# Performance work log

Measured on AMD Instinct MI355X. Metric: run time of the kernel, lower is better.

## Reference

```python
import jax, jax.numpy as jnp
import numpy as np
from jax import lax

# encoder config from the module: (out_ch, kernel, stride), 3x3, padding=1 (pytlib ConvolutionStack)
_LAYERS = [(3, 3, 2), (16, 3, 2), (64, 3, 1), (128, 3, 2), (256, 3, 1)]
_DN = ('NCHW', 'OIHW', 'NCHW')


def _make_params(key):
    params = []
    in_ch = 3
    for i, (out_ch, k, _s) in enumerate(_LAYERS):
        kw, kb = jax.random.split(jax.random.fold_in(key, i))
        fan_in = in_ch * k * k
        W = jax.random.normal(kw, (out_ch, in_ch, k, k), jnp.float32) * np.sqrt(2.0 / fan_in)
        b = jnp.zeros((out_ch,), jnp.float32)
        params.append((W, b))
        in_ch = out_ch
    return params


def _encoder(x, W0, b0, W1, b1, W2, b2, W3, b3, W4, b4):
    Ws = (W0, W1, W2, W3, W4)
    bs = (b0, b1, b2, b3, b4)
    for i, (_oc, _k, s) in enumerate(_LAYERS):
        x = lax.conv_general_dilated(x, Ws[i], (s, s), ((1, 1), (1, 1)), dimension_numbers=_DN)
        x = x + bs[i][None, :, None, None]
        if i < len(_LAYERS) - 1:  # final_relu=False
            x = jax.nn.relu(x)
    return x


def setup_inputs() -> dict:
    key = jax.random.key(0)
    k1, k2, kp = jax.random.split(key, 3)
    crop = jax.random.normal(k1, (64, 3, 64, 64), jnp.float32)
    frame = jax.random.normal(k2, (64, 3, 256, 256), jnp.float32)
    params = _make_params(kp)
    out = {'crop': crop, 'frame': frame}
    for i, (W, b) in enumerate(params):
        out[f'W{i}'] = W
        out[f'b{i}'] = b
    out['gamma'] = jnp.ones((1,), jnp.float32)
    out['beta'] = jnp.zeros((1,), jnp.float32)
    return out


def reference(crop, frame, W0, b0, W1, b1, W2, b2, W3, b3, W4, b4, gamma, beta):
    crop_fm = _encoder(crop, W0, b0, W1, b1, W2, b2, W3, b3, W4, b4)   # [B,256,8,8]
    frame_fm = _encoder(frame, W0, b0, W1, b1, W2, b2, W3, b3, W4, b4)  # [B,256,32,32]

    # per-sample cross-correlation: crop feature map is the conv kernel (vectorized over batch)
    def xcorr(f, k):  # f:[C,H,W], k:[C,h,w] -> [1,Hr,Wr]
        return lax.conv_general_dilated(f[None], k[None], (1, 1), 'VALID', dimension_numbers=_DN)[0]

    rmap = jax.vmap(xcorr)(frame_fm, crop_fm)  # [B,1,25,25]

    # BatchNorm2d(1), training mode: batch stats over (N,H,W), biased variance, eps=1e-5
    mean = jnp.mean(rmap, axis=(0, 2, 3), keepdims=True)
    var = jnp.mean(jnp.square(rmap - mean), axis=(0, 2, 3), keepdims=True)
    rmap = (rmap - mean) * lax.rsqrt(var + 1e-5)
    rmap = rmap * gamma[None, :, None, None] + beta[None, :, None, None]
    return rmap
```

## Files before the change

### kernel.cpp

```cpp
#include <hip/hip_runtime.h>


typedef __bf16 bf16x8 __attribute__((ext_vector_type(8)));
typedef float f32x4 __attribute__((ext_vector_type(4)));
typedef unsigned int u32x4 __attribute__((ext_vector_type(4)));
typedef unsigned int u32x2 __attribute__((ext_vector_type(2)));
typedef unsigned short u16;

#define AS1 __attribute__((address_space(1)))
#define AS3 __attribute__((address_space(3)))

__device__ __forceinline__ u16 f2bf(float v) {
    unsigned u = __float_as_uint(v);
    u += 0x7fffu + ((u >> 16) & 1u);
    return (u16)(u >> 16);
}

__device__ __forceinline__ bf16x8 ldb8(const u16* p) {
    return *(const bf16x8*)p;
}

__device__ __forceinline__ bf16x8 zerob8() {
    u32x4 z = {0u, 0u, 0u, 0u};
    bf16x8 r;
    __builtin_memcpy(&r, &z, 16);
    return r;
}

__device__ __forceinline__ void gload16(const u16* g, u16* l) {
    __builtin_amdgcn_global_load_lds((const AS1 void*)g, (AS3 void*)l, 16, 0, 0);
}

template<int N> __device__ __forceinline__ void wait_vm() {
    asm volatile("s_waitcnt vmcnt(%0)" :: "i"(N) : "memory");
}

__device__ __forceinline__ void bar_mem() {
    asm volatile("" ::: "memory");
    __builtin_amdgcn_s_barrier();
    asm volatile("" ::: "memory");
}

struct CP { const u16* in; u16* out; int IWp, inSS, OWsh, OWpo, outSS, npt; };
struct CQ { const u16* in; u16* out; int IWp, inSS, HWsh, OWsh, OWpo, outSS, pad_o; };

struct HZd { unsigned long long ptr; int B, Hp, Wpx, w8, cum; };
struct HZall { HZd d[8]; int total; };

__global__ __launch_bounds__(256)
void haloz_k(HZall h)
{
    for (int i = blockIdx.x * 256 + threadIdx.x; i < h.total; i += gridDim.x * 256) {
        int di = 0;
        #pragma unroll
        for (int j = 1; j < 8; ++j) if (i >= h.d[j].cum) di = j;
        const HZd D = h.d[di];
        const int loc = i - D.cum;
        const int w = loc % D.w8; int t2 = loc / D.w8;
        const int bord = 2 * D.Wpx + 2 * (D.Hp - 2);
        const int pb = t2 % bord; const int b = t2 / bord;
        int oh, ow;
        if (pb < D.Wpx)            { oh = 0;        ow = pb; }
        else if (pb < 2 * D.Wpx)   { oh = D.Hp - 1; ow = pb - D.Wpx; }
        else { const int q = pb - 2 * D.Wpx; oh = 1 + (q >> 1); ow = (q & 1) ? (D.Wpx - 1) : 0; }
        ((unsigned long long*)D.ptr)[((size_t)b * D.Hp * D.Wpx + (size_t)oh * D.Wpx + ow) * D.w8 + w] = 0ull;
    }
}

__device__ __forceinline__ void packone(const float* W, u16* Wp, int idx,
                                        int ICsh, int Kpad)
{
    const int k = idx % Kpad, oc = idx / Kpad;
    const int tap = k >> ICsh, ic = k & ((1 << ICsh) - 1);
    const float v = (tap < 9) ? W[((size_t)(oc << ICsh) + ic) * 9 + tap] : 0.f;
    Wp[idx] = f2bf(v);
}

__global__ __launch_bounds__(256)
void packall_k(const float* __restrict__ W1, const float* __restrict__ W2,
               const float* __restrict__ W3, const float* __restrict__ W4,
               u16* __restrict__ Wc1, u16* __restrict__ Wp2,
               u16* __restrict__ Wp3, u16* __restrict__ Wp4)
{
    const int i = blockIdx.x * 256 + threadIdx.x;
    if (i < 1024) {
        const int k = i & 63, oc = i >> 6;
        const int ky = k >> 4, kx = (k >> 2) & 3, ic = k & 3;
        const float v = (ky < 3 && kx < 3 && ic < 3) ? W1[oc * 27 + ic * 9 + ky * 3 + kx] : 0.f;
        Wc1[i] = f2bf(v);
    } else if (i < 11264) {
        packone(W2, Wp2, i - 1024, 4, 160);
    } else if (i < 84992) {
        packone(W3, Wp3, i - 11264, 6, 576);
    } else if (i < 379904) {
        packone(W4, Wp4, i - 84992, 7, 1152);
    }
}

__device__ __forceinline__ void conv0_body(const float* __restrict__ in,
                                           const float* __restrict__ W,
                                           const float* __restrict__ bias,
                                           u16* __restrict__ outP,
                                           int IH, int IW, int OH, int OW, int idx)
{
    const int OW4 = OW >> 2;
    const int OWp = OW + 2, OHp = OH + 2;
    const int ow4 = idx % OW4; int t = idx / OW4;
    const int oh = t % OH;  const int b = t / OH;
    const int owb = ow4 * 4;
    float a0[4], a1[4], a2[4];
    #pragma unroll
    for (int j = 0; j < 4; ++j) { a0[j] = bias[0]; a1[j] = bias[1]; a2[j] = bias[2]; }
    const float* inb = in + (size_t)b * 3 * IH * IW;
    const int xbase = owb * 2 - 1;
    #pragma unroll
    for (int ic = 0; ic < 3; ++ic) {
        const float* ip = inb + (size_t)ic * IH * IW;
        #pragma unroll
        for (int ky = 0; ky < 3; ++ky) {
            const int y = oh * 2 - 1 + ky;
            if ((unsigned)y >= (unsigned)IH) continue;
            const float* rp = ip + (size_t)y * IW;
            float xr[9];
            #pragma unroll
            for (int i2 = 0; i2 < 9; ++i2) {
                const int x = xbase + i2;
                xr[i2] = ((unsigned)x < (unsigned)IW) ? rp[x] : 0.f;
            }
            #pragma unroll
            for (int kx = 0; kx < 3; ++kx) {
                const float w0 = W[0 * 27 + ic * 9 + ky * 3 + kx];
                const float w1 = W[1 * 27 + ic * 9 + ky * 3 + kx];
                const float w2 = W[2 * 27 + ic * 9 + ky * 3 + kx];
                #pragma unroll
                for (int j = 0; j < 4; ++j) {
                    const float xv = xr[2 * j + kx];
                    a0[j] += xv * w0; a1[j] += xv * w1; a2[j] += xv * w2;
                }
            }
        }
    }
    u16* op = outP + (((size_t)b * OHp + oh + 1) * OWp + owb + 1) * 4;
    #pragma unroll
    for (int j = 0; j < 4; ++j) {
        u32x2 pk;
        pk[0] = (unsigned)f2bf(fmaxf(a0[j], 0.f)) | ((unsigned)f2bf(fmaxf(a1[j], 0.f)) << 16);
        pk[1] = (unsigned)f2bf(fmaxf(a2[j], 0.f));
        *(u32x2*)(op + j * 4) = pk;
    }
}

__global__ __launch_bounds__(256)
void conv0m_k(const float* __restrict__ crop, const float* __restrict__ frame,
              const float* __restrict__ W, const float* __restrict__ bias,
              u16* __restrict__ c0b, u16* __restrict__ f0b)
{
    if (blockIdx.x < 64)
        conv0_body(crop, W, bias, c0b, 64, 64, 32, 32, blockIdx.x * 256 + threadIdx.x);
    else
        conv0_body(frame, W, bias, f0b, 256, 256, 128, 128, (blockIdx.x - 64) * 256 + threadIdx.x);
}

__device__ __forceinline__ void conv1g_body(const u16* __restrict__ inP,
                                            const u16* __restrict__ Wc1,
                                            const float* __restrict__ bias,
                                            u16* __restrict__ outP,
                                            int IWp, int inSS, int OWp, int outSS,
                                            int OWsh, int HWsh, int w, int lane)
{
    const int lr = lane & 15, lg = lane >> 4;
    const int pxb = w * 64;
    const int OW = 1 << OWsh;

    const bf16x8 av0 = ldb8(Wc1 + lr * 64 + lg * 8);
    const bf16x8 av1 = ldb8(Wc1 + lr * 64 + 32 + lg * 8);
    const int ky0 = lg >> 1, kxb = (lg & 1) * 2;
    const int ky1 = 2 + (lg >> 1);

    f32x4 acc[4] = {};
    #pragma unroll
    for (int n = 0; n < 4; ++n) {
        const int px = pxb + n * 16 + lr;
        const int b = px >> HWsh;
        const int rem = px & ((1 << HWsh) - 1);
        const int oh = rem >> OWsh, ow = rem & (OW - 1);
        const u16* ib = inP + (size_t)b * inSS + (((size_t)(oh * 2)) * IWp + ow * 2) * 4;
        const bf16x8 bv0 = ldb8(ib + ((size_t)ky0 * IWp + kxb) * 4);
        acc[n] = __builtin_amdgcn_mfma_f32_16x16x32_bf16(av0, bv0, acc[n], 0, 0, 0);
        const bf16x8 bv1 = ldb8(ib + ((size_t)ky1 * IWp + kxb) * 4);
        acc[n] = __builtin_amdgcn_mfma_f32_16x16x32_bf16(av1, bv1, acc[n], 0, 0, 0);
    }

    const float b0 = bias[lg * 4], b1 = bias[lg * 4 + 1],
                b2 = bias[lg * 4 + 2], b3 = bias[lg * 4 + 3];
    #pragma unroll
    for (int n = 0; n < 4; ++n) {
        const int px = pxb + n * 16 + lr;
        const int b = px >> HWsh;
        const int rem = px & ((1 << HWsh) - 1);
        const int oh = rem >> OWsh, ow = rem & (OW - 1);
        const f32x4 a = acc[n];
        u32x2 pk;
        pk[0] = (unsigned)f2bf(fmaxf(a[0] + b0, 0.f)) | ((unsigned)f2bf(fmaxf(a[1] + b1, 0.f)) << 16);
        pk[1] = (unsigned)f2bf(fmaxf(a[2] + b2, 0.f)) | ((unsigned)f2bf(fmaxf(a[3] + b3, 0.f)) << 16);
        u16* op = outP + (size_t)b * outSS + (((size_t)(oh + 1)) * OWp + (ow + 1)) * 16 + lg * 4;
        *(u32x2*)op = pk;
    }
}

__global__ __launch_bounds__(256)
void conv1m_k(const u16* __restrict__ c0b, u16* __restrict__ c1p,
              const u16* __restrict__ f0b, u16* __restrict__ f1p,
              const u16* __restrict__ Wc1, const float* __restrict__ bias)
{
    const int wv = threadIdx.x >> 6, lane = threadIdx.x & 63;
    if (blockIdx.x < 64)
        conv1g_body(c0b, Wc1, bias, c1p, 34, 4624, 18, 5184, 4, 8, blockIdx.x * 4 + wv, lane);
    else
        conv1g_body(f0b, Wc1, bias, f1p, 130, 67600, 66, 69696, 6, 12, (blockIdx.x - 64) * 4 + wv, lane);
}

template<int BM, int BN, int NWM, int NWN, int S>
__global__ __launch_bounds__(512, 4)
void convq3_k(CQ F, CQ C, int splitPt, int nmt_sh,
              const u16* __restrict__ Wp, const float* __restrict__ bias,
              int IC_sh, int nt, int Kpad, int relu, int OCt)
{
    constexpr int MF = BM / (NWM * 16);
    constexpr int NF = BN / (NWN * 16);
    constexpr int AH = BM * 4 / 512;
    constexpr int BH = BN * 4 / 512;
    constexpr int WAIT  = 2 * AH + BH;
    constexpr int TAIL0 = AH + BH;
    constexpr int ASZ = 2 * 2 * BM * 4 * 8;
    constexpr int BSZ = 2 * 2 * BN * 4 * 8;

    __shared__ __align__(16) u16 SM[ASZ + BSZ];
    u16* Ab = SM;
    u16* Bb = SM + ASZ;

    const int mt  = blockIdx.x & ((1 << nmt_sh) - 1);
    const int ptg = blockIdx.x >> nmt_sh;
    CQ P; int pt;
    if (ptg < splitPt) { P = F; pt = ptg; }
    else               { P = C; pt = ptg - splitPt; }
    const int ocb = mt * BM;

    const int t    = threadIdx.x;
    const int lane = t & 63;
    const int lr   = lane & 15, lg = lane >> 4;
    const int wv   = t >> 6;
    const int wm   = wv / NWN, wn = wv % NWN;

    const int IC = 1 << IC_sh;
    const int OW = 1 << P.OWsh;
    const int HWm = (1 << P.HWsh) - 1;
    const int pxb = pt * BN;

    const u16* apg[2 * AH];
    #pragma unroll
    for (int h = 0; h < 2; ++h)
        #pragma unroll
        for (int i = 0; i < AH; ++i) {
            const int j = i * 512 + t;
            const int row = j >> 2, o = j & 3;
            const int oct = h * 4 + (o ^ ((row ^ (row >> 2)) & 3));
            apg[h * AH + i] = Wp + (size_t)(ocb + row) * Kpad + oct * 8;
        }
    const u16* bpg[2 * BH];
    #pragma unroll
    for (int h = 0; h < 2; ++h)
        #pragma unroll
        for (int i = 0; i < BH; ++i) {
            const int j = i * 512 + t;
            const int row = j >> 2, o = j & 3;
            const int oct = h * 4 + (o ^ ((row ^ (row >> 2)) & 3));
            const int px = pxb + row;
            const int b = px >> P.HWsh;
            const int rem = px & HWm;
            const int oh = rem >> P.OWsh, ow = rem & (OW - 1);
            bpg[h * BH + i] = P.in + (size_t)b * P.inSS
                            + ((size_t)(oh * S) * P.IWp + ow * S) * IC + oct * 8;
        }

    f32x4 acc[MF][NF] = {};

    auto STAGE_A = [&](int buf, int h, int kb) {
        u16* dst = Ab + (size_t)((buf * 2 + h) * BM * 4) * 8;
        #pragma unroll
        for (int i = 0; i < AH; ++i)
            gload16(apg[h * AH + i] + kb, dst + (size_t)(i * 512 + t) * 8);
    };
    auto STAGE_B = [&](int buf, int h, int kb) {
        const int tap = kb >> IC_sh;
        const int ky = (tap * 11) >> 5, kx = tap - 3 * ky;
        const size_t off = ((size_t)(ky * P.IWp + kx) << IC_sh) + (kb & (IC - 1));
        u16* dst = Bb + (size_t)((buf * 2 + h) * BN * 4) * 8;
        #pragma unroll
        for (int i = 0; i < BH; ++i)
            gload16(bpg[h * BH + i] + off, dst + (size_t)(i * 512 + t) * 8);
    };

    STAGE_A(0, 0, 0); STAGE_B(0, 0, 0); STAGE_A(0, 1, 0); STAGE_B(0, 1, 0);

    for (int ks = 0; ks < nt; ++ks) {
        const int cur = ks & 1, nxt = cur ^ 1;
        const int kb1 = (ks + 1) * 64;
        const bool pf = (ks + 1 < nt);
        bf16x8 af[MF], bf_[NF];

        #pragma unroll
        for (int kk = 0; kk < 2; ++kk) {
            if (pf) STAGE_A(nxt, kk, kb1);
            if (pf)            wait_vm<WAIT>();
            else if (kk == 0)  wait_vm<TAIL0>();
            else               wait_vm<0>();
            bar_mem();

            const u16* Abase = Ab + (size_t)((cur * 2 + kk) * BM * 4) * 8;
            const u16* Bbase = Bb + (size_t)((cur * 2 + kk) * BN * 4) * 8;
            #pragma unroll
            for (int n = 0; n < NF; ++n) {
                const int row = wn * (NF * 16) + n * 16 + lr;
                const int o = lg ^ ((row ^ (row >> 2)) & 3);
                bf_[n] = ldb8(Bbase + (size_t)(row * 4 + o) * 8);
            }
            #pragma unroll
            for (int m = 0; m < MF; ++m) {
                const int row = wm * (MF * 16) + m * 16 + lr;
                const int o = lg ^ ((row ^ (row >> 2)) & 3);
                af[m] = ldb8(Abase + (size_t)(row * 4 + o) * 8);
            }
            if (pf) STAGE_B(nxt, kk, kb1);

            __builtin_amdgcn_s_setprio(1);
            #pragma unroll
            for (int m = 0; m < MF; ++m)
                #pragma unroll
                for (int n = 0; n < NF; ++n)
                    acc[m][n] = __builtin_amdgcn_mfma_f32_16x16x32_bf16(af[m], bf_[n], acc[m][n], 0, 0, 0);
            __builtin_amdgcn_s_setprio(0);
        }
    }

    bar_mem();
    unsigned long long* SM64 = (unsigned long long*)SM;
    #pragma unroll
    for (int m = 0; m < MF; ++m) {
        const int ocl = wm * (MF * 16) + m * 16 + lg * 4;
        const float b0 = bias[ocb + ocl], b1 = bias[ocb + ocl + 1],
                    b2 = bias[ocb + ocl + 2], b3 = bias[ocb + ocl + 3];
        #pragma unroll
        for (int n = 0; n < NF; ++n) {
            const int px = wn * (NF * 16) + n * 16 + lr;
            const f32x4 a = acc[m][n];
            float v0 = a[0] + b0, v1 = a[1] + b1, v2 = a[2] + b2, v3 = a[3] + b3;
            if (relu) {
                v0 = fmaxf(v0, 0.f); v1 = fmaxf(v1, 0.f);
                v2 = fmaxf(v2, 0.f); v3 = fmaxf(v3, 0.f);
            }
            u32x2 pk;
            pk[0] = (unsigned)f2bf(v0) | ((unsigned)f2bf(v1) << 16);
            pk[1] = (unsigned)f2bf(v2) | ((unsigned)f2bf(v3) << 16);
            const int sw = ((px & 3) << 1) | ((px >> 2) & 1);
            const int u8 = (ocl >> 2) ^ (sw << 1);
            *(u32x2*)&SM64[(size_t)px * (BM / 4) + u8] = pk;
        }
    }
    bar_mem();
    constexpr int UPX16 = BM / 8;
    constexpr int NIT = BN * UPX16 / 512;
    #pragma unroll
    for (int it = 0; it < NIT; ++it) {
        const int g = it * 512 + t;
        const int px = g / UPX16;
        const int ul = g & (UPX16 - 1);
        const int sw = ((px & 3) << 1) | ((px >> 2) & 1);
        const int phys = ul ^ sw;
        const u32x4 val = *(const u32x4*)&SM[((size_t)px * UPX16 + phys) * 8];
        const int flat = pxb + px;
        const int b = flat >> P.HWsh;
        const int rem = flat & HWm;
        const int oh = rem >> P.OWsh, ow = rem & (OW - 1);
        u16* dst = P.out + (size_t)b * P.outSS
                 + (((size_t)(oh + P.pad_o)) * P.OWpo + (ow + P.pad_o)) * OCt
                 + ocb + ul * 8;
        *(u32x4*)dst = val;
    }
}

template<int BM, int BN, int NWM, int NWN, int S>
__global__ __launch_bounds__(256, 2)
void convg3_k(CP A, CP B, int split,
              const u16* __restrict__ Wp, const float* __restrict__ bias,
              int IC_sh, int pad_o, int Kreal, int nt, int Kpad, int relu, int OCtot)
{
    constexpr int MF = BM / (NWM * 16);
    constexpr int NF = BN / (NWN * 16);
    constexpr int ASLOT = BM * 4;
    constexpr int BSLOT = BN * 4;
    constexpr int AISS = ASLOT / 256;
    constexpr int BISS = BSLOT / 256;
    constexpr int NSTG = AISS + BISS;

    __shared__ __align__(16) u16 Ab[4][ASLOT * 8];
    __shared__ __align__(16) u16 Bb[4][BSLOT * 8];

    CP P; int bid;
    if (blockIdx.x < (unsigned)split) { P = A; bid = blockIdx.x; }
    else                              { P = B; bid = blockIdx.x - split; }

    const int t    = threadIdx.x;
    const int wv   = t >> 6, lane = t & 63;
    const int lr   = lane & 15, lg = lane >> 4;
    const int wm   = wv / NWN, wn = wv % NWN;

    const int tilesPerB = (OCtot / BM) * P.npt;
    const int b  = bid / tilesPerB;
    const int r0 = bid - b * tilesPerB;
    const int mt = r0 / P.npt, pt = r0 - mt * P.npt;
    const int ocb = mt * BM, pxb = pt * BN;
    const int IC = 1 << IC_sh;
    const int OW = 1 << P.OWsh;

    const u16* __restrict__ inb = P.in + (size_t)b * P.inSS;

    const u16* agp[AISS];
    #pragma unroll
    for (int i = 0; i < AISS; ++i) {
        const int s = i * 256 + t;
        const int q = s / BM, rr = s - q * BM;
        agp[i] = Wp + (size_t)(ocb + rr) * Kpad + q * 8;
    }
    int bq[BISS]; const u16* bpx[BISS];
    #pragma unroll
    for (int i = 0; i < BISS; ++i) {
        const int s = i * 256 + t;
        const int q = s / BN, rr = s - q * BN;
        const int px = pxb + rr;
        const int oh = px >> P.OWsh, ow = px & (OW - 1);
        bq[i] = q;
        bpx[i] = inb + ((size_t)(oh * S) * P.IWp + ow * S) * IC;
    }

    f32x4 acc[MF][NF] = {};

    auto STAGE = [&](int buf, int kb) {
        #pragma unroll
        for (int i = 0; i < AISS; ++i)
            gload16(agp[i] + kb, &Ab[buf][(size_t)(i * 256 + wv * 64) * 8]);
        #pragma unroll
        for (int i = 0; i < BISS; ++i) {
            const int k = kb + bq[i] * 8;
            const int tap = k >> IC_sh;
            const int ic = k & (IC - 1);
            const int ky = (tap * 11) >> 5, kx = tap - 3 * ky;
            const u16* g = bpx[i] + ((size_t)ky * P.IWp + kx) * IC + ic;
            if (k >= Kreal) g = inb;
            gload16(g, &Bb[buf][(size_t)(i * 256 + wv * 64) * 8]);
        }
    };

    STAGE(0, 0);
    if (1 < nt) STAGE(1, 32);
    if (2 < nt) STAGE(2, 64);

    for (int ks = 0; ks < nt; ++ks) {
        const int rem = nt - 1 - ks;
        if (rem >= 2)      wait_vm<2 * NSTG>();
        else if (rem == 1) wait_vm<NSTG>();
        else               wait_vm<0>();
        bar_mem();
        if (ks + 3 < nt) STAGE((ks + 3) & 3, (ks + 3) * 32);

        const int cur = ks & 3;
        bf16x8 af[MF], bf_[NF];
        #pragma unroll
        for (int m = 0; m < MF; ++m)
            af[m] = ldb8(&Ab[cur][(size_t)(lg * BM + wm * (MF * 16) + m * 16 + lr) * 8]);
        #pragma unroll
        for (int n = 0; n < NF; ++n)
            bf_[n] = ldb8(&Bb[cur][(size_t)(lg * BN + wn * (NF * 16) + n * 16 + lr) * 8]);

        __builtin_amdgcn_s_setprio(1);
        #pragma unroll
        for (int m = 0; m < MF; ++m)
            #pragma unroll
            for (int n = 0; n < NF; ++n)
                acc[m][n] = __builtin_amdgcn_mfma_f32_16x16x32_bf16(af[m], bf_[n], acc[m][n], 0, 0, 0);
        __builtin_amdgcn_s_setprio(0);
    }

    #pragma unroll
    for (int m = 0; m < MF; ++m) {
        const int oc0 = ocb + wm * (MF * 16) + m * 16 + lg * 4;
        const float b0 = bias[oc0], b1 = bias[oc0 + 1], b2 = bias[oc0 + 2], b3 = bias[oc0 + 3];
        #pragma unroll
        for (int n = 0; n < NF; ++n) {
            const int px = pxb + wn * (NF * 16) + n * 16 + lr;
            const int oh = px >> P.OWsh, ow = px & (OW - 1);
            const f32x4 a = acc[m][n];
            float v0 = a[0] + b0, v1 = a[1] + b1, v2 = a[2] + b2, v3 = a[3] + b3;
            if (relu) {
                v0 = fmaxf(v0, 0.f); v1 = fmaxf(v1, 0.f);
                v2 = fmaxf(v2, 0.f); v3 = fmaxf(v3, 0.f);
            }
            u32x2 pk;
            pk[0] = (unsigned)f2bf(v0) | ((unsigned)f2bf(v1) << 16);
            pk[1] = (unsigned)f2bf(v2) | ((unsigned)f2bf(v3) << 16);
            u16* op = P.out + (size_t)b * P.outSS +
                      (((size_t)(oh + pad_o)) * P.OWpo + (ow + pad_o)) * (size_t)OCtot + oc0;
            *(u32x2*)op = pk;
        }
    }
}

__global__ __launch_bounds__(256)
void xcmf_k(const u16* __restrict__ ffm, const u16* __restrict__ cfm,
            float* __restrict__ R)
{
    const int w    = blockIdx.x * 4 + (threadIdx.x >> 6);
    const int lane = threadIdx.x & 63;
    const int lr   = lane & 15, lg = lane >> 4;
    const int b  = w / 25;
    const int tp = w - b * 25;

    const int col0 = tp * 32 + lr;
    const int col1 = col0 + 16;
    const int y0 = col0 / 25, x0 = col0 - y0 * 25;
    const int y1 = col1 / 25, x1 = col1 - y1 * 25;

    const u16* fb = ffm + (size_t)b * 262144;
    const u16* f0 = fb + ((size_t)y0 * 32 + x0) * 256 + lg * 8;
    const u16* f1 = fb + ((size_t)y1 * 32 + x1) * 256 + lg * 8;
    const u16* ab = cfm + (size_t)b * 16384 + (size_t)lr * 2048 + lg * 8;
    const bool arow = (lr < 8);

    f32x4 acc0 = {}, acc1 = {};
    #pragma unroll 4
    for (int kb = 0; kb < 2048; kb += 32) {
        const bf16x8 av = arow ? ldb8(ab + kb) : zerob8();
        const bf16x8 bv0 = ldb8(f0 + kb);
        const bf16x8 bv1 = ldb8(f1 + kb);
        acc0 = __builtin_amdgcn_mfma_f32_16x16x32_bf16(av, bv0, acc0, 0, 0, 0);
        acc1 = __builtin_amdgcn_mfma_f32_16x16x32_bf16(av, bv1, acc1, 0, 0, 0);
    }

    if (lg < 2) {
        float* rb = R + (size_t)b * 6400;
        #pragma unroll
        for (int j = 0; j < 4; ++j) {
            const int d = lg * 4 + j;
            rb[(size_t)d * 800 + col0] = acc0[j];
            rb[(size_t)d * 800 + col1] = acc1[j];
        }
    }
}

__global__ __launch_bounds__(1024)
void bn_k(const float* __restrict__ R, float* __restrict__ part,
          const float* __restrict__ gamma, const float* __restrict__ beta,
          float* __restrict__ out)
{
    const int N = 40000;
    const int tid = threadIdx.x;
    __shared__ float rs[1024], rq[1024];
    __shared__ float mean_s, inv_s;
    float s = 0.f, q = 0.f;
    for (int i = tid; i < N; i += 1024) {
        const int b = i / 625;
        const int o = i - b * 625;
        const float* rb = R + (size_t)b * 6400 + o;
        float v = 0.f;
        #pragma unroll
        for (int d = 0; d < 8; ++d) v += rb[(size_t)d * 800 + d * 25];
        part[i] = v;
        s += v; q += v * v;
    }
    rs[tid] = s; rq[tid] = q;
    __syncthreads();
    for (int off = 512; off > 0; off >>= 1) {
        if (tid < off) { rs[tid] += rs[tid + off]; rq[tid] += rq[tid + off]; }
        __syncthreads();
    }
    if (tid == 0) {
        const float m = rs[0] / (float)N;
        mean_s = m;
        inv_s = rsqrtf(rq[0] / (float)N - m * m + 1e-5f);
    }
    __syncthreads();
    const float g = gamma[0], bt = beta[0];
    for (int i = tid; i < N; i += 1024)
        out[i] = (part[i] - mean_s) * inv_s * g + bt;
}


extern "C" void kernel_launch(void* const* d_in, const int* in_sizes, int n_in,
                              void* d_out, int out_size, void* d_ws, size_t ws_size,
                              hipStream_t stream)
{
    (void)in_sizes; (void)n_in; (void)out_size; (void)ws_size;
    const float* crop  = (const float*)d_in[0];
    const float* frame = (const float*)d_in[1];
    const float* W[5]; const float* bb[5];
    for (int i = 0; i < 5; ++i) { W[i] = (const float*)d_in[2 + 2*i]; bb[i] = (const float*)d_in[3 + 2*i]; }
    const float* gamma = (const float*)d_in[12];
    const float* beta  = (const float*)d_in[13];
    float* out = (float*)d_out;

    unsigned char* ws = (unsigned char*)d_ws;
    u16*   f0b  = (u16*)(ws + 0);
    u16*   f1p  = (u16*)(ws + 8652800);
    u16*   f2p  = (u16*)(ws + 17573888);
    u16*   f3p  = (u16*)(ws + 53258240);
    u16*   ffm  = (u16*)(ws + 0);
    u16*   c0b  = (u16*)(ws + 72198144);
    u16*   c1p  = (u16*)(ws + 72790016);
    u16*   c2p  = (u16*)(ws + 73453568);
    u16*   c3p  = (u16*)(ws + 76107776);
    u16*   cfm  = (u16*)(ws + 77746176);
    u16*   Wc1  = (u16*)(ws + 79843328);
    u16*   Wp2  = (u16*)(ws + 79845376);
    u16*   Wp3  = (u16*)(ws + 79865856);
    u16*   Wp4  = (u16*)(ws + 80013312);
    float* Rbuf = (float*)(ws + 80603136);
    float* part = (float*)(ws + 82241536);

    HZall hz;
    const unsigned long long ptrs[8] = {(unsigned long long)c0b, (unsigned long long)c1p,
        (unsigned long long)c2p, (unsigned long long)c3p, (unsigned long long)f0b,
        (unsigned long long)f1p, (unsigned long long)f2p, (unsigned long long)f3p};
    const int Hps[8] = {34, 18, 18, 10, 130, 66, 66, 34};
    const int w8s[8] = {1, 4, 16, 32, 1, 4, 16, 32};
    int cum = 0;
    for (int i = 0; i < 8; ++i) {
        hz.d[i].ptr = ptrs[i]; hz.d[i].B = 64; hz.d[i].Hp = Hps[i];
        hz.d[i].Wpx = Hps[i]; hz.d[i].w8 = w8s[i]; hz.d[i].cum = cum;
        cum += 64 * (2 * Hps[i] + 2 * (Hps[i] - 2)) * w8s[i];
    }
    hz.total = cum;
    haloz_k<<<1024, 256, 0, stream>>>(hz);

    packall_k<<<1484, 256, 0, stream>>>(W[1], W[2], W[3], W[4], Wc1, Wp2, Wp3, Wp4);

    conv0m_k<<<1088, 256, 0, stream>>>(crop, frame, W[0], bb[0], c0b, f0b);
    conv1m_k<<<1088, 256, 0, stream>>>(c0b, c1p, f0b, f1p, Wc1, bb[1]);
    {
        CP Ac = {c1p, c2p, 18,  5184, 4, 18, 20736,  1};
        CP Bf = {f1p, f2p, 66, 69696, 6, 66, 278784, 16};
        convg3_k<64,256,1,4,1><<<1088, 256, 0, stream>>>(Ac, Bf, 64, Wp2, bb[2],
            4, 1, 144, 5, 160, 1, 64);
    }

    {
        CQ F3 = {f2p, f3p, 66, 278784, 10,  5,   34,  147968, 1};
        CQ C3 = {c2p, c3p, 18,  20736,  6,  3,   10,   12800, 1};
        convq3_k<128,128,2,4,2><<< 544, 512, 0, stream>>>(F3, C3, 512, 0, Wp3, bb[3], 6,  9,  576, 1, 128);
        CQ F4 = {f3p, ffm, 34, 147968, 10,  5,   32,  262144, 0};
        CQ C4 = {c3p, cfm, 10,  12800,  6,  3,    8,   16384, 0};
        convq3_k<128,128,2,4,1><<<1088, 512, 0, stream>>>(F4, C4, 512, 1, Wp4, bb[4], 7, 18, 1152, 0, 256);
    }

    xcmf_k<<<400, 256, 0, stream>>>(ffm, cfm, Rbuf);
    bn_k<<<1, 1024, 0, stream>>>(Rbuf, part, gamma, beta, out);
}
```

Measured before the change: 230.7 us.

## Fuse prep kernels, remap blocks per XCD, swizzle LDS layout in convg

Merges the halo-zeroing and weight-packing kernels into one launch, which removes one kernel launch. Remaps block indices in the two GEMM conv kernels so that consecutive logical tiles land on the same XCD, aiming for better L2 reuse of weights and inputs. Changes the convg LDS staging layout to a row-major layout with an XOR swizzle, intended to cut LDS bank conflicts on the MFMA operand reads. The XCD remap assumes the grid size is divisible by 8, which holds for 1088 and 544.

Result: no change. 227.5 us (-1.4%).

```diff
diff --git a/kernel.cpp b/kernel.cpp
--- a/kernel.cpp
+++ b/kernel.cpp
@@ -41,16 +41,51 @@
     asm volatile("" ::: "memory");
 }
 
+__device__ __forceinline__ int xcd_logical() {
+    const int nb = (int)gridDim.x;
+    return ((int)blockIdx.x & 7) * (nb >> 3) + ((int)blockIdx.x >> 3);
+}
+
 struct CP { const u16* in; u16* out; int IWp, inSS, OWsh, OWpo, outSS, npt; };
 struct CQ { const u16* in; u16* out; int IWp, inSS, HWsh, OWsh, OWpo, outSS, pad_o; };
 
 struct HZd { unsigned long long ptr; int B, Hp, Wpx, w8, cum; };
 struct HZall { HZd d[8]; int total; };
 
+__device__ __forceinline__ void packone(const float* W, u16* Wp, int idx,
+                                        int ICsh, int Kpad)
+{
+    const int k = idx % Kpad, oc = idx / Kpad;
+    const int tap = k >> ICsh, ic = k & ((1 << ICsh) - 1);
+    const float v = (tap < 9) ? W[((size_t)(oc << ICsh) + ic) * 9 + tap] : 0.f;
+    Wp[idx] = f2bf(v);
+}
+
 __global__ __launch_bounds__(256)
-void haloz_k(HZall h)
-{
-    for (int i = blockIdx.x * 256 + threadIdx.x; i < h.total; i += gridDim.x * 256) {
+void prep_k(HZall h,
+            const float* __restrict__ W1, const float* __restrict__ W2,
+            const float* __restrict__ W3, const float* __restrict__ W4,
+            u16* __restrict__ Wc1, u16* __restrict__ Wp2,
+            u16* __restrict__ Wp3, u16* __restrict__ Wp4)
+{
+    if (blockIdx.x < 1484) {
+        const int i = blockIdx.x * 256 + threadIdx.x;
+        if (i < 1024) {
+            const int k = i & 63, oc = i >> 6;
+            const int ky = k >> 4, kx = (k >> 2) & 3, ic = k & 3;
+            const float v = (ky < 3 && kx < 3 && ic < 3) ? W1[oc * 27 + ic * 9 + ky * 3 + kx] : 0.f;
+            Wc1[i] = f2bf(v);
+        } else if (i < 11264) {
+            packone(W2, Wp2, i - 1024, 4, 160);
+        } else if (i < 84992) {
+            packone(W3, Wp3, i - 11264, 6, 576);
+        } else if (i < 379904) {
+            packone(W4, Wp4, i - 84992, 7, 1152);
+        }
+        return;
+    }
+    const int nblk = gridDim.x - 1484;
+    for (int i = (blockIdx.x - 1484) * 256 + threadIdx.x; i < h.total; i += nblk * 256) {
         int di = 0;
         #pragma unroll
         for (int j = 1; j < 8; ++j) if (i >= h.d[j].cum) di = j;
@@ -64,36 +99,6 @@
         else if (pb < 2 * D.Wpx)   { oh = D.Hp - 1; ow = pb - D.Wpx; }
         else { const int q = pb - 2 * D.Wpx; oh = 1 + (q >> 1); ow = (q & 1) ? (D.Wpx - 1) : 0; }
         ((unsigned long long*)D.ptr)[((size_t)b * D.Hp * D.Wpx + (size_t)oh * D.Wpx + ow) * D.w8 + w] = 0ull;
-    }
-}
-
-__device__ __forceinline__ void packone(const float* W, u16* Wp, int idx,
-                                        int ICsh, int Kpad)
-{
-    const int k = idx % Kpad, oc = idx / Kpad;
-    const int tap = k >> ICsh, ic = k & ((1 << ICsh) - 1);
-    const float v = (tap < 9) ? W[((size_t)(oc << ICsh) + ic) * 9 + tap] : 0.f;
-    Wp[idx] = f2bf(v);
-}
-
-__global__ __launch_bounds__(256)
-void packall_k(const float* __restrict__ W1, const float* __restrict__ W2,
-               const float* __restrict__ W3, const float* __restrict__ W4,
-               u16* __restrict__ Wc1, u16* __restrict__ Wp2,
-               u16* __restrict__ Wp3, u16* __restrict__ Wp4)
-{
-    const int i = blockIdx.x * 256 + threadIdx.x;
-    if (i < 1024) {
-        const int k = i & 63, oc = i >> 6;
-        const int ky = k >> 4, kx = (k >> 2) & 3, ic = k & 3;
-        const float v = (ky < 3 && kx < 3 && ic < 3) ? W1[oc * 27 + ic * 9 + ky * 3 + kx] : 0.f;
-        Wc1[i] = f2bf(v);
-    } else if (i < 11264) {
-        packone(W2, Wp2, i - 1024, 4, 160);
-    } else if (i < 84992) {
-        packone(W3, Wp3, i - 11264, 6, 576);
-    } else if (i < 379904) {
-        packone(W4, Wp4, i - 84992, 7, 1152);
     }
 }
 
@@ -239,8 +244,9 @@
     u16* Ab = SM;
     u16* Bb = SM + ASZ;
 
-    const int mt  = blockIdx.x & ((1 << nmt_sh) - 1);
-    const int ptg = blockIdx.x >> nmt_sh;
+    const int lbid = xcd_logical();
+    const int mt  = lbid & ((1 << nmt_sh) - 1);
+    const int ptg = lbid >> nmt_sh;
     CQ P; int pt;
     if (ptg < splitPt) { P = F; pt = ptg; }
     else               { P = C; pt = ptg - splitPt; }
@@ -391,7 +397,7 @@
 
 template<int BM, int BN, int NWM, int NWN, int S>
 __global__ __launch_bounds__(256, 2)
-void convg3_k(CP A, CP B, int split,
+void convg4_k(CP A, CP B, int split,
               const u16* __restrict__ Wp, const float* __restrict__ bias,
               int IC_sh, int pad_o, int Kreal, int nt, int Kpad, int relu, int OCtot)
 {
@@ -406,9 +412,10 @@
     __shared__ __align__(16) u16 Ab[4][ASLOT * 8];
     __shared__ __align__(16) u16 Bb[4][BSLOT * 8];
 
+    const int lbid = xcd_logical();
     CP P; int bid;
-    if (blockIdx.x < (unsigned)split) { P = A; bid = blockIdx.x; }
-    else                              { P = B; bid = blockIdx.x - split; }
+    if (lbid < split) { P = A; bid = lbid; }
+    else              { P = B; bid = lbid - split; }
 
     const int t    = threadIdx.x;
     const int wv   = t >> 6, lane = t & 63;
@@ -428,19 +435,21 @@
     const u16* agp[AISS];
     #pragma unroll
     for (int i = 0; i < AISS; ++i) {
-        const int s = i * 256 + t;
-        const int q = s / BM, rr = s - q * BM;
-        agp[i] = Wp + (size_t)(ocb + rr) * Kpad + q * 8;
-    }
-    int bq[BISS]; const u16* bpx[BISS];
+        const int j = i * 256 + t;
+        const int row = j >> 2, c = j & 3;
+        const int og = c ^ ((row ^ (row >> 2)) & 3);
+        agp[i] = Wp + (size_t)(ocb + row) * Kpad + og * 8;
+    }
+    const u16* bpx[BISS]; int bog8[BISS];
     #pragma unroll
     for (int i = 0; i < BISS; ++i) {
-        const int s = i * 256 + t;
-        const int q = s / BN, rr = s - q * BN;
-        const int px = pxb + rr;
+        const int j = i * 256 + t;
+        const int row = j >> 2, c = j & 3;
+        const int og = c ^ ((row ^ (row >> 2)) & 3);
+        const int px = pxb + row;
         const int oh = px >> P.OWsh, ow = px & (OW - 1);
-        bq[i] = q;
         bpx[i] = inb + ((size_t)(oh * S) * P.IWp + ow * S) * IC;
+        bog8[i] = og * 8;
     }
 
     f32x4 acc[MF][NF] = {};
@@ -448,16 +457,16 @@
     auto STAGE = [&](int buf, int kb) {
         #pragma unroll
         for (int i = 0; i < AISS; ++i)
-            gload16(agp[i] + kb, &Ab[buf][(size_t)(i * 256 + wv * 64) * 8]);
+            gload16(agp[i] + kb, &Ab[buf][(size_t)(i * 256 + t) * 8]);
         #pragma unroll
         for (int i = 0; i < BISS; ++i) {
-            const int k = kb + bq[i] * 8;
+            const int k = kb + bog8[i];
             const int tap = k >> IC_sh;
             const int ic = k & (IC - 1);
             const int ky = (tap * 11) >> 5, kx = tap - 3 * ky;
             const u16* g = bpx[i] + ((size_t)ky * P.IWp + kx) * IC + ic;
             if (k >= Kreal) g = inb;
-            gload16(g, &Bb[buf][(size_t)(i * 256 + wv * 64) * 8]);
+            gload16(g, &Bb[buf][(size_t)(i * 256 + t) * 8]);
         }
     };
 
@@ -476,11 +485,17 @@
         const int cur = ks & 3;
         bf16x8 af[MF], bf_[NF];
         #pragma unroll
-        for (int m = 0; m < MF; ++m)
-            af[m] = ldb8(&Ab[cur][(size_t)(lg * BM + wm * (MF * 16) + m * 16 + lr) * 8]);
-        #pragma unroll
-        for (int n = 0; n < NF; ++n)
-            bf_[n] = ldb8(&Bb[cur][(size_t)(lg * BN + wn * (NF * 16) + n * 16 + lr) * 8]);
+        for (int m = 0; m < MF; ++m) {
+            const int row = wm * (MF * 16) + m * 16 + lr;
+            const int o = lg ^ ((row ^ (row >> 2)) & 3);
+            af[m] = ldb8(&Ab[cur][(size_t)(row * 4 + o) * 8]);
+        }
+        #pragma unroll
+        for (int n = 0; n < NF; ++n) {
+            const int row = wn * (NF * 16) + n * 16 + lr;
+            const int o = lg ^ ((row ^ (row >> 2)) & 3);
+            bf_[n] = ldb8(&Bb[cur][(size_t)(row * 4 + o) * 8]);
+        }
 
         __builtin_amdgcn_s_setprio(1);
         #pragma unroll
@@ -639,16 +654,14 @@
         cum += 64 * (2 * Hps[i] + 2 * (Hps[i] - 2)) * w8s[i];
     }
     hz.total = cum;
-    haloz_k<<<1024, 256, 0, stream>>>(hz);
-
-    packall_k<<<1484, 256, 0, stream>>>(W[1], W[2], W[3], W[4], Wc1, Wp2, Wp3, Wp4);
+    prep_k<<<1856, 256, 0, stream>>>(hz, W[1], W[2], W[3], W[4], Wc1, Wp2, Wp3, Wp4);
 
     conv0m_k<<<1088, 256, 0, stream>>>(crop, frame, W[0], bb[0], c0b, f0b);
     conv1m_k<<<1088, 256, 0, stream>>>(c0b, c1p, f0b, f1p, Wc1, bb[1]);
     {
         CP Ac = {c1p, c2p, 18,  5184, 4, 18, 20736,  1};
         CP Bf = {f1p, f2p, 66, 69696, 6, 66, 278784, 16};
-        convg3_k<64,256,1,4,1><<<1088, 256, 0, stream>>>(Ac, Bf, 64, Wp2, bb[2],
+        convg4_k<64,256,1,4,1><<<1088, 256, 0, stream>>>(Ac, Bf, 64, Wp2, bb[2],
             4, 1, 144, 5, 160, 1, 64);
     }
 
```
